# Optimization experiments

Measured on AMD Instinct MI355X. Metric: run time of the kernel, lower is better.

Reference implementation:

```python
import jax, jax.numpy as jnp
import numpy as np

B, S, D = 4, 2048, 1024
H = 16
HD = D // H
DFF = 4096
MAX_REL = 32
EPS = 1e-5


def _rms_norm(x, w):
    rms = jnp.sqrt(jnp.mean(x * x, axis=-1, keepdims=True) + EPS)
    return x / rms * w


def setup_inputs() -> dict:
    key = jax.random.key(0)
    ks = jax.random.split(key, 16)
    sc = 0.02
    d = {
        "x": jax.random.normal(ks[0], (B, S, D), dtype=jnp.float32),
        "g1": jnp.ones((D,), dtype=jnp.float32),
        "g2": jnp.ones((D,), dtype=jnp.float32),
        "wq": jax.random.normal(ks[1], (D, D), dtype=jnp.float32) * sc,
        "bq": jnp.zeros((D,), dtype=jnp.float32),
        "wk": jax.random.normal(ks[2], (D, D), dtype=jnp.float32) * sc,
        "bk": jnp.zeros((D,), dtype=jnp.float32),
        "wv": jax.random.normal(ks[3], (D, D), dtype=jnp.float32) * sc,
        "bv": jnp.zeros((D,), dtype=jnp.float32),
        "wo": jax.random.normal(ks[4], (D, D), dtype=jnp.float32) * sc,
        "bo": jnp.zeros((D,), dtype=jnp.float32),
        "rel_pos": jax.random.normal(ks[5], (H, 2 * MAX_REL + 1), dtype=jnp.float32),
        "w1": jax.random.normal(ks[6], (D, DFF), dtype=jnp.float32) * sc,
        "b1": jnp.zeros((DFF,), dtype=jnp.float32),
        "w2": jax.random.normal(ks[7], (DFF, D), dtype=jnp.float32) * sc,
        "b2": jnp.zeros((D,), dtype=jnp.float32),
    }
    return d


def reference(x, g1, g2, wq, bq, wk, bk, wv, bv, wo, bo, rel_pos, w1, b1, w2, b2):
    b, s, d = x.shape
    # --- multi-head attention with relative-position bias ---
    q = (x @ wq + bq).reshape(b, s, H, HD).transpose(0, 2, 1, 3)  # [B,H,S,HD]
    k = (x @ wk + bk).reshape(b, s, H, HD).transpose(0, 2, 1, 3)
    v = (x @ wv + bv).reshape(b, s, H, HD).transpose(0, 2, 1, 3)
    scores = jnp.einsum("bhqd,bhkd->bhqk", q, k) / jnp.sqrt(jnp.float32(HD))
    # relative position bias: gather from (H, 2*MAX_REL+1) table
    pos = jnp.arange(s)
    rel = pos[None, :] - pos[:, None]                # [S,S]
    idx = jnp.clip(rel, -MAX_REL, MAX_REL) + MAX_REL  # [S,S]
    bias = rel_pos[:, idx]                            # [H,S,S]
    scores = scores + bias[None]
    attn = jax.nn.softmax(scores, axis=-1)
    out = jnp.einsum("bhqk,bhkd->bhqd", attn, v)
    out = out.transpose(0, 2, 1, 3).reshape(b, s, d)
    attn_out = out @ wo + bo
    # residual + RMSNorm
    x = _rms_norm(attn_out + x, g1)
    # --- feed-forward (exact GELU) ---
    h = jax.nn.gelu(x @ w1 + b1, approximate=False)
    ff = h @ w2 + b2
    x = _rms_norm(ff + x, g2)
    return x
```

## Files before the change

### kernel.cpp

```cpp
#include <hip/hip_runtime.h>

#define B_ 4
#define S_ 2048
#define D_ 1024
#define H_ 16
#define HD_ 64
#define DFF_ 4096
#define MR_ 32
#define M_ (B_*S_)

typedef unsigned short u16;
typedef __attribute__((ext_vector_type(8))) short bf16x8;
typedef __attribute__((ext_vector_type(4))) float f32x4;

#define MFMA16 __builtin_amdgcn_mfma_f32_16x16x32_bf16
#define A_CONST 0.18033688011112f
#define LOG2E_ 1.44269504088896f

__device__ __forceinline__ u16 f2b(float f) {
  unsigned u = __builtin_bit_cast(unsigned, f);
  u = u + 0x7FFFu + ((u >> 16) & 1u);
  return (u16)(u >> 16);
}
__device__ __forceinline__ float b2f(u16 h) {
  unsigned u = ((unsigned)h) << 16;
  return __builtin_bit_cast(float, u);
}
__device__ __forceinline__ float exp2_fast(float x) {
  float r;
  asm("v_exp_f32 %0, %1" : "=v"(r) : "v"(x));
  return r;
}
__device__ __forceinline__ unsigned cvtpk(float lo, float hi) {
  unsigned r;
  asm("v_cvt_pk_bf16_f32 %0, %1, %2" : "=v"(r) : "v"(lo), "v"(hi));
  return r;
}
__device__ __forceinline__ float max3f(float a, float b, float c) {
  float r;
  asm("v_max3_f32 %0, %1, %2, %3" : "=v"(r) : "v"(a), "v"(b), "v"(c));
  return r;
}
__device__ __forceinline__ int med3i(int a, int b, int c) {
  int r;
  asm("v_med3_i32 %0, %1, %2, %3" : "=v"(r) : "v"(a), "v"(b), "v"(c));
  return r;
}
__device__ __forceinline__ void gl_lds16(const void* g, void* l) {
  __builtin_amdgcn_global_load_lds(
      (const __attribute__((address_space(1))) void*)g,
      (__attribute__((address_space(3))) void*)l, 16, 0, 0);
}

#define SWZ(r) ((((((r)>>3)&1)<<2) ^ ((r)&7)) << 4)
#define SWZ64(r) ((((r)>>1)&3) << 4)

__global__ __launch_bounds__(256) void cvt_kernel(const float* __restrict__ in,
                                                  u16* __restrict__ out, int n4) {
  int i = blockIdx.x * 256 + threadIdx.x;
  if (i < n4) {
    float4 v = ((const float4*)in)[i];
    ushort4 o;
    o.x = f2b(v.x); o.y = f2b(v.y); o.z = f2b(v.z); o.w = f2b(v.w);
    ((ushort4*)out)[i] = o;
  }
}

__global__ __launch_bounds__(256) void wtrans_kernel(const float* __restrict__ in,
                                                     u16* __restrict__ out, int R, int C) {
  __shared__ float t[32][33];
  int c0 = blockIdx.x * 32, r0 = blockIdx.y * 32;
  int x = threadIdx.x, y = threadIdx.y;
#pragma unroll
  for (int i = 0; i < 4; ++i)
    t[y + i*8][x] = in[(long)(r0 + y + i*8) * C + c0 + x];
  __syncthreads();
#pragma unroll
  for (int i = 0; i < 4; ++i)
    out[(long)(c0 + y + i*8) * R + r0 + x] = f2b(t[x][y + i*8]);
}

__global__ __launch_bounds__(256) void vtrans_kernel(const u16* __restrict__ v,
                                                     u16* __restrict__ vT) {
  __shared__ u16 t[32][33];
  int bh = blockIdx.y; int b = bh >> 4, h = bh & 15;
  int s0 = (blockIdx.x >> 1) * 32;
  int d0 = (blockIdx.x & 1) * 32;
  int x = threadIdx.x, y = threadIdx.y;
#pragma unroll
  for (int i = 0; i < 4; ++i)
    t[y + i*8][x] = v[((long)(b*S_ + s0 + y + i*8)) * D_ + h*64 + d0 + x];
  __syncthreads();
#pragma unroll
  for (int i = 0; i < 4; ++i)
    vT[((long)((b*H_ + h)*HD_ + d0 + y + i*8)) * S_ + s0 + x] = t[x][y + i*8];
}

template<int EPI, int WN>
__global__ __launch_bounds__(512, 2) void gemm9(
    const u16* __restrict__ A, const u16* __restrict__ BT,
    const float* __restrict__ bias0, const float* __restrict__ bias1,
    const float* __restrict__ bias2,
    u16* __restrict__ C0, u16* __restrict__ C1, u16* __restrict__ C2,
    int Ndim, int Kdim)
{
  constexpr int BN = WN * 64;
  constexpr int WM = 8 / WN;
  constexpr int MROWS = 256 / WM;
  constexpr int MF = MROWS / 16;
  __shared__ char lds[4][32768];
  const int tid = threadIdx.x;
  const int w = tid >> 6, lane = tid & 63;
  const int lr = lane & 15, lg = lane >> 4;
  const int wm = w / WN, wn = w % WN;

  const int nbx = Ndim / BN;
  const int cpx = gridDim.x >> 3;
  const int bid = blockIdx.x;
  const int swzb = (bid & 7) * cpx + (bid >> 3);
  const long blockM = (long)(swzb / nbx) * 256;
  const long blockN = (long)(swzb % nbx) * BN;

  const int srow = tid >> 2;
  const int scol = ((tid & 3) * 16) ^ SWZ64(srow);
  const u16* Ag  = A + (blockM + srow) * (long)Kdim + (scol >> 1);
  const u16* Ag2 = Ag + (long)128 * Kdim;
  const u16* Bg  = BT + (blockN + srow) * (long)Kdim + (scol >> 1);
  const u16* Bg2 = Bg + (long)128 * Kdim;
  char* const ldsAw = &lds[0][0] + w * 1024;
  char* const ldsBw = &lds[0][0] + 16384 + w * 1024;

#define STAGE_A(t) { char* d_=ldsAw+((t)&3)*32768; const long ko_=(long)(t)*32; \
    gl_lds16(Ag  + ko_, d_); gl_lds16(Ag2 + ko_, d_ + 8192); }
#define STAGE_B(t) { char* d_=ldsBw+((t)&3)*32768; const long ko_=(long)(t)*32; \
    gl_lds16(Bg  + ko_, d_); if constexpr (WN==4) gl_lds16(Bg2 + ko_, d_ + 8192); }

  const int rsw = (lg * 16) ^ SWZ64(lr);
  int offA[MF], offB[4];
#pragma unroll
  for (int mf = 0; mf < MF; ++mf) offA[mf] = (wm*MROWS + mf*16 + lr) * 64 + rsw;
#pragma unroll
  for (int nf = 0; nf < 4; ++nf)  offB[nf] = 16384 + (wn*64 + nf*16 + lr) * 64 + rsw;

  f32x4 acc[MF][4] = {};
  const int NS = Kdim >> 5;

  STAGE_A(0); STAGE_B(0); STAGE_A(1); STAGE_B(1);
  if (WN == 4) asm volatile("s_waitcnt vmcnt(4)" ::: "memory");
  else         asm volatile("s_waitcnt vmcnt(3)" ::: "memory");
  __builtin_amdgcn_s_barrier();

  for (int t = 0; t < NS; ++t) {
    const char* sl = &lds[t & 3][0];
    bf16x8 af[MF], bfr[4];
    if constexpr (WN == 4) {
#pragma unroll
      for (int mf = 0; mf < MF; ++mf) af[mf] = *(const bf16x8*)(sl + offA[mf]);
      bfr[0] = *(const bf16x8*)(sl + offB[0]);
      bfr[1] = *(const bf16x8*)(sl + offB[1]);
      if (t + 2 < NS) STAGE_A(t + 2);
      __builtin_amdgcn_s_barrier();
      __builtin_amdgcn_s_setprio(1);
#pragma unroll
      for (int mf = 0; mf < MF; ++mf) acc[mf][0] = MFMA16(bfr[0], af[mf], acc[mf][0], 0, 0, 0);
#pragma unroll
      for (int mf = 0; mf < MF; ++mf) acc[mf][1] = MFMA16(bfr[1], af[mf], acc[mf][1], 0, 0, 0);
      __builtin_amdgcn_s_setprio(0);
      __builtin_amdgcn_s_barrier();
      bfr[2] = *(const bf16x8*)(sl + offB[2]);
      bfr[3] = *(const bf16x8*)(sl + offB[3]);
      if (t + 2 < NS) {
        STAGE_B(t + 2);
        asm volatile("s_waitcnt vmcnt(4)" ::: "memory");
      } else if (t == NS - 2) {
        asm volatile("s_waitcnt vmcnt(0)" ::: "memory");
      }
      __builtin_amdgcn_s_barrier();
      __builtin_amdgcn_s_setprio(1);
#pragma unroll
      for (int mf = 0; mf < MF; ++mf) acc[mf][2] = MFMA16(bfr[2], af[mf], acc[mf][2], 0, 0, 0);
#pragma unroll
      for (int mf = 0; mf < MF; ++mf) acc[mf][3] = MFMA16(bfr[3], af[mf], acc[mf][3], 0, 0, 0);
      __builtin_amdgcn_s_setprio(0);
      __builtin_amdgcn_s_barrier();
    } else {
#pragma unroll
      for (int mf = 0; mf < MF; ++mf) af[mf] = *(const bf16x8*)(sl + offA[mf]);
#pragma unroll
      for (int nf = 0; nf < 4; ++nf)  bfr[nf] = *(const bf16x8*)(sl + offB[nf]);
      if (t + 2 < NS) {
        STAGE_A(t + 2); STAGE_B(t + 2);
        asm volatile("s_waitcnt vmcnt(3)" ::: "memory");
      } else if (t == NS - 2) {
        asm volatile("s_waitcnt vmcnt(0)" ::: "memory");
      }
      __builtin_amdgcn_s_barrier();
      __builtin_amdgcn_s_setprio(1);
#pragma unroll
      for (int mf = 0; mf < MF; ++mf)
#pragma unroll
        for (int nf = 0; nf < 4; ++nf)
          acc[mf][nf] = MFMA16(bfr[nf], af[mf], acc[mf][nf], 0, 0, 0);
      __builtin_amdgcn_s_setprio(0);
      __builtin_amdgcn_s_barrier();
    }
  }

  const float* bsel = bias0;
  u16* osel = C0;
  long nstride = Ndim;
  long ncol0 = blockN;
  if (EPI == 3) {
    int mat = (int)(blockN >> 10);
    bsel = mat == 0 ? bias0 : (mat == 1 ? bias1 : bias2);
    osel = mat == 0 ? C0 : (mat == 1 ? C1 : C2);
    nstride = 1024;
    ncol0 = blockN & 1023;
  }
  const long row0 = blockM + wm*MROWS;
#pragma unroll
  for (int mf = 0; mf < MF; ++mf) {
    long row = row0 + mf*16 + lr;
#pragma unroll
    for (int nf = 0; nf < 4; ++nf) {
      long col = ncol0 + wn*64 + nf*16 + lg*4;
      float4 bv = *(const float4*)&bsel[col];
      float v0 = acc[mf][nf][0] + bv.x;
      float v1 = acc[mf][nf][1] + bv.y;
      float v2 = acc[mf][nf][2] + bv.z;
      float v3 = acc[mf][nf][3] + bv.w;
      if (EPI == 2) {
        v0 = 0.5f*v0*(1.0f + erff(v0*0.70710678118654752f));
        v1 = 0.5f*v1*(1.0f + erff(v1*0.70710678118654752f));
        v2 = 0.5f*v2*(1.0f + erff(v2*0.70710678118654752f));
        v3 = 0.5f*v3*(1.0f + erff(v3*0.70710678118654752f));
      }
      ushort4 st;
      st.x = f2b(v0); st.y = f2b(v1); st.z = f2b(v2); st.w = f2b(v3);
      *(ushort4*)&osel[row * nstride + col] = st;
    }
  }
#undef STAGE_A
#undef STAGE_B
}

__device__ __forceinline__ float max16v(const f32x4* s) {
  float a = max3f(s[0][0], s[0][1], s[0][2]);
  float b = max3f(s[0][3], s[1][0], s[1][1]);
  float c = max3f(s[1][2], s[1][3], s[2][0]);
  float d = max3f(s[2][1], s[2][2], s[2][3]);
  float e = max3f(s[3][0], s[3][1], s[3][2]);
  float f = max3f(a, b, s[3][3]);
  float g = max3f(c, d, e);
  return fmaxf(f, g);
}
__device__ __forceinline__ float max16s(const float* v) {
  float a = max3f(v[0], v[1], v[2]);
  float b = max3f(v[3], v[4], v[5]);
  float c = max3f(v[6], v[7], v[8]);
  float d = max3f(v[9], v[10], v[11]);
  float e = max3f(v[12], v[13], v[14]);
  float f = max3f(a, b, v[15]);
  float g = max3f(c, d, e);
  return fmaxf(f, g);
}

__device__ __forceinline__ void sm_finish(float* p, float& l_r, bf16x8* pfo) {
  float ls = ((p[0]+p[1])+(p[2]+p[3])) + ((p[4]+p[5])+(p[6]+p[7]))
           + ((p[8]+p[9])+(p[10]+p[11])) + ((p[12]+p[13])+(p[14]+p[15]));
  ls += __shfl_xor(ls, 16);
  ls += __shfl_xor(ls, 32);
  l_r += ls;
#pragma unroll
  for (int ks = 0; ks < 2; ++ks) {
    uint4 uu;
    uu.x = cvtpk(p[ks*4+0], p[ks*4+1]);
    uu.y = cvtpk(p[ks*4+2], p[ks*4+3]);
    uu.z = cvtpk(p[(ks+2)*4+0], p[(ks+2)*4+1]);
    uu.w = cvtpk(p[(ks+2)*4+2], p[(ks+2)*4+3]);
    pfo[ks] = __builtin_bit_cast(bf16x8, uu);
  }
}

__device__ __forceinline__ void softmax_uni(const f32x4* s, float bu,
    float& m_r, float& l_r, f32x4* acc, bf16x8* pfo)
{
  float mx = fmaf(max16v(s), A_CONST, bu);
  mx = fmaxf(mx, __shfl_xor(mx, 16));
  mx = fmaxf(mx, __shfl_xor(mx, 32));
  if (!__all(mx <= m_r + 8.0f)) {
    float mn = fmaxf(m_r, mx);
    float sc = exp2_fast(m_r - mn);
    m_r = mn;
    l_r *= sc;
#pragma unroll
    for (int ni = 0; ni < 4; ++ni) acc[ni] *= sc;
  }
  float cc = bu - m_r;
  float p[16];
#pragma unroll
  for (int ni = 0; ni < 4; ++ni)
#pragma unroll
    for (int j = 0; j < 4; ++j)
      p[ni*4+j] = exp2_fast(fmaf(s[ni][j], A_CONST, cc));
  sm_finish(p, l_r, pfo);
}

__device__ __forceinline__ void softmax_slow(const f32x4* s, const float* relb,
    int rbase, float& m_r, float& l_r, f32x4* acc, bf16x8* pfo)
{
  float sv[16];
#pragma unroll
  for (int ni = 0; ni < 4; ++ni) {
    const int koff = (ni&1)*32 + (ni>>1)*4;
#pragma unroll
    for (int j = 0; j < 4; ++j) {
      int idx = med3i(rbase + koff + j + MR_, 0, 2*MR_);
      sv[ni*4+j] = fmaf(s[ni][j], A_CONST, relb[idx]);
    }
  }
  float mx = max16s(sv);
  mx = fmaxf(mx, __shfl_xor(mx, 16));
  mx = fmaxf(mx, __shfl_xor(mx, 32));
  if (!__all(mx <= m_r + 8.0f)) {
    float mn = fmaxf(m_r, mx);
    float sc = exp2_fast(m_r - mn);
    m_r = mn;
    l_r *= sc;
#pragma unroll
    for (int ni = 0; ni < 4; ++ni) acc[ni] *= sc;
  }
  float p[16];
#pragma unroll
  for (int i = 0; i < 16; ++i) p[i] = exp2_fast(sv[i] - m_r);
  sm_finish(p, l_r, pfo);
}

__global__ __launch_bounds__(256, 4) void attn3_kernel(
    const u16* __restrict__ q, const u16* __restrict__ k,
    const u16* __restrict__ vT, const float* __restrict__ rel_pos,
    u16* __restrict__ ao)
{
  __shared__ u16 KB[2][4096];
  __shared__ u16 VB[2][4096];
  __shared__ float relb[2*MR_ + 1];

  const int tid = threadIdx.x;
  const int w = tid >> 6, lane = tid & 63;
  const int lr = lane & 15, lg = lane >> 4;
  const int qt = blockIdx.x, bh = blockIdx.y;
  const int b = bh >> 4, h = bh & 15;
  const int q0 = qt * 128;
  const int qq = q0 + w*32;

  if (tid < 2*MR_ + 1) relb[tid] = rel_pos[h * (2*MR_ + 1) + tid] * LOG2E_;

  const int srow0 = w*8 + (lane >> 3);
  const int srow1 = 32 + srow0;
  const int scb   = (lane & 7) * 16;
  const int col0  = scb ^ SWZ(srow0);
  const int col1  = scb ^ SWZ(srow1);

  const long qkbase = ((long)(b*S_)) * D_ + h*64;
  const long vbase  = ((long)((b*H_ + h) * HD_)) * S_;

  {
    const u16* qg = q + qkbase + (long)q0 * D_;
#pragma unroll
    for (int c = 0; c < 4; ++c) {
      int row = c*32 + srow0;
      int colc = scb ^ SWZ(row);
      gl_lds16(qg + (long)row*D_ + (colc >> 1), &KB[0][0] + (c*32 + w*8)*64);
    }
  }
  __syncthreads();
  bf16x8 qf[4];
#pragma unroll
  for (int qi = 0; qi < 2; ++qi)
#pragma unroll
    for (int ks = 0; ks < 2; ++ks) {
      int row = w*32 + qi*16 + lr;
      qf[qi*2+ks] = *(const bf16x8*)((const char*)&KB[0][0] + row*128 + ((ks*64 + lg*16) ^ SWZ(row)));
    }
  const float bHI = relb[2*MR_];
  const float bLO = relb[0];
  __syncthreads();

  int offK0[4], offV0[4];
#pragma unroll
  for (int ni = 0; ni < 4; ++ni) {
    int kr = (ni&1)*32 + (lr>>2)*8 + (ni>>1)*4 + (lr&3);
    int vr = ni*16 + lr;
    offK0[ni] = kr*128 + ((lg*16) ^ SWZ(kr));
    offV0[ni] = vr*128 + ((lg*16) ^ SWZ(vr));
  }

  const u16* kp0 = k  + qkbase + (long)srow0*D_ + (col0 >> 1);
  const u16* kp1 = k  + qkbase + (long)srow1*D_ + (col1 >> 1);
  const u16* vp0 = vT + vbase  + (long)srow0*S_ + (col0 >> 1);
  const u16* vp1 = vT + vbase  + (long)srow1*S_ + (col1 >> 1);
  u16* kb_w0 = &KB[0][(w*8)*64];
  u16* kb_w1 = &KB[0][(32 + w*8)*64];
  u16* vb_w0 = &VB[0][(w*8)*64];
  u16* vb_w1 = &VB[0][(32 + w*8)*64];

  float m_r[2] = {-1e30f, -1e30f};
  float l_r[2] = {0.f, 0.f};
  f32x4 acco[2][4] = {};

  gl_lds16(kp0, kb_w0);
  gl_lds16(kp1, kb_w1);
  gl_lds16(vp0, vb_w0);
  gl_lds16(vp1, vb_w1);

  const long kstep = (long)64 * D_;
  const int NT = S_ / 64;
  for (int t = 0; t < NT; ++t) {
    const int cur = t & 1;
    __syncthreads();
    if (t + 1 < NT) {
      int bufo = (cur ^ 1) * 4096;
      gl_lds16(kp0 + (long)(t+1)*kstep, kb_w0 + bufo);
      gl_lds16(kp1 + (long)(t+1)*kstep, kb_w1 + bufo);
      gl_lds16(vp0 + (t+1)*64, vb_w0 + bufo);
      gl_lds16(vp1 + (t+1)*64, vb_w1 + bufo);
    }
    const char* Kb = (const char*)&KB[cur][0];
    const char* Vb = (const char*)&VB[cur][0];
    const int k0 = t * 64;

    f32x4 s0[4] = {}, s1[4] = {};
#pragma unroll
    for (int ks = 0; ks < 2; ++ks)
#pragma unroll
      for (int ni = 0; ni < 4; ++ni) {
        bf16x8 kf = *(const bf16x8*)(Kb + (offK0[ni] ^ (ks*64)));
        s0[ni] = MFMA16(kf, qf[ks],   s0[ni], 0, 0, 0);
        s1[ni] = MFMA16(kf, qf[2+ks], s1[ni], 0, 0, 0);
      }

    bf16x8 pf0[2], pf1[2];
    bool hi_u = (k0 - (qq + 31)) >= MR_;
    bool lo_u = (qq - (k0 + 63)) >= MR_;
    if (hi_u || lo_u) {
      float bu = hi_u ? bHI : bLO;
      softmax_uni(s0, bu, m_r[0], l_r[0], acco[0], pf0);
      softmax_uni(s1, bu, m_r[1], l_r[1], acco[1], pf1);
    } else {
      int rb0 = k0 + lg*8 - (qq + lr);
      softmax_slow(s0, relb, rb0,      m_r[0], l_r[0], acco[0], pf0);
      softmax_slow(s1, relb, rb0 - 16, m_r[1], l_r[1], acco[1], pf1);
    }

#pragma unroll
    for (int ks = 0; ks < 2; ++ks)
#pragma unroll
      for (int ni = 0; ni < 4; ++ni) {
        bf16x8 vf = *(const bf16x8*)(Vb + (offV0[ni] ^ (ks*64)));
        acco[0][ni] = MFMA16(vf, pf0[ks], acco[0][ni], 0, 0, 0);
        acco[1][ni] = MFMA16(vf, pf1[ks], acco[1][ni], 0, 0, 0);
      }
  }

#pragma unroll
  for (int qi = 0; qi < 2; ++qi) {
    float inv = 1.0f / l_r[qi];
    long orow = ((long)(b*S_ + qq + qi*16 + lr)) * D_ + h*64;
#pragma unroll
    for (int ni = 0; ni < 4; ++ni) {
      ushort4 ov;
      ov.x = f2b(acco[qi][ni][0] * inv);
      ov.y = f2b(acco[qi][ni][1] * inv);
      ov.z = f2b(acco[qi][ni][2] * inv);
      ov.w = f2b(acco[qi][ni][3] * inv);
      *(ushort4*)(ao + orow + ni*16 + lg*4) = ov;
    }
  }
}

template<int ABF, int BBF>
__global__ __launch_bounds__(256) void rmsnorm_kernel(
    const void* __restrict__ a, const void* __restrict__ b,
    const float* __restrict__ g, float* __restrict__ outf,
    u16* __restrict__ outb)
{
  long row = blockIdx.x;
  int tid = threadIdx.x;
  float ya[4], yb[4], y[4];
  if (ABF) {
    ushort4 av = ((const ushort4*)a)[row*256 + tid];
    ya[0] = b2f(av.x); ya[1] = b2f(av.y); ya[2] = b2f(av.z); ya[3] = b2f(av.w);
  } else {
    float4 av = ((const float4*)a)[row*256 + tid];
    ya[0] = av.x; ya[1] = av.y; ya[2] = av.z; ya[3] = av.w;
  }
  if (BBF) {
    ushort4 bv = ((const ushort4*)b)[row*256 + tid];
    yb[0] = b2f(bv.x); yb[1] = b2f(bv.y); yb[2] = b2f(bv.z); yb[3] = b2f(bv.w);
  } else {
    float4 bv = ((const float4*)b)[row*256 + tid];
    yb[0] = bv.x; yb[1] = bv.y; yb[2] = bv.z; yb[3] = bv.w;
  }
  float ss = 0.f;
#pragma unroll
  for (int i = 0; i < 4; ++i) { y[i] = ya[i] + yb[i]; ss += y[i]*y[i]; }
#pragma unroll
  for (int m = 1; m < 64; m <<= 1) ss += __shfl_xor(ss, m);
  __shared__ float red[4];
  int w = tid >> 6, lane = tid & 63;
  if (lane == 0) red[w] = ss;
  __syncthreads();
  ss = red[0] + red[1] + red[2] + red[3];
  float rinv = rsqrtf(ss * (1.0f / D_) + 1e-5f);
  float4 gv = ((const float4*)g)[tid];
  float o[4] = { y[0]*rinv*gv.x, y[1]*rinv*gv.y, y[2]*rinv*gv.z, y[3]*rinv*gv.w };
  if (outf) {
    float4 of = { o[0], o[1], o[2], o[3] };
    ((float4*)outf)[row*256 + tid] = of;
  }
  if (outb) {
    ushort4 ob;
    ob.x = f2b(o[0]); ob.y = f2b(o[1]); ob.z = f2b(o[2]); ob.w = f2b(o[3]);
    ((ushort4*)outb)[row*256 + tid] = ob;
  }
}

extern "C" void kernel_launch(void* const* d_in, const int* in_sizes, int n_in,
                              void* d_out, int out_size, void* d_ws, size_t ws_size,
                              hipStream_t stream) {
  const float* x   = (const float*)d_in[0];
  const float* g1  = (const float*)d_in[1];
  const float* g2  = (const float*)d_in[2];
  const float* wq  = (const float*)d_in[3];
  const float* bq  = (const float*)d_in[4];
  const float* wk  = (const float*)d_in[5];
  const float* bk  = (const float*)d_in[6];
  const float* wv  = (const float*)d_in[7];
  const float* bv  = (const float*)d_in[8];
  const float* wo  = (const float*)d_in[9];
  const float* bo  = (const float*)d_in[10];
  const float* rel = (const float*)d_in[11];
  const float* w1  = (const float*)d_in[12];
  const float* b1  = (const float*)d_in[13];
  const float* w2  = (const float*)d_in[14];
  const float* b2  = (const float*)d_in[15];
  float* out = (float*)d_out;

  char* ws = (char*)d_ws;
  const size_t MB = 1024ull * 1024ull;
  u16* xb   = (u16*)(ws + 0);
  u16* wqT  = (u16*)(ws + 16*MB);
  u16* wkT  = (u16*)(ws + 18*MB);
  u16* wvT  = (u16*)(ws + 20*MB);
  u16* woT  = (u16*)(ws + 22*MB);
  u16* w1T  = (u16*)(ws + 24*MB);
  u16* w2T  = (u16*)(ws + 32*MB);
  u16* qb   = (u16*)(ws + 40*MB);
  u16* kb   = (u16*)(ws + 56*MB);
  u16* vb   = (u16*)(ws + 72*MB);
  u16* vTb  = (u16*)(ws + 88*MB);
  u16* aob  = (u16*)(ws + 104*MB);
  u16* prjb = (u16*)(ws + 120*MB);
  u16* x1b  = (u16*)(ws + 136*MB);
  u16* hb   = (u16*)(ws + 40*MB);
  u16* ffb  = (u16*)(ws + 120*MB);
  (void)ws_size; (void)in_sizes; (void)n_in; (void)out_size;

  dim3 tb(32, 8);

  cvt_kernel<<<M_*D_/4/256, 256, 0, stream>>>(x, xb, M_*D_/4);
  wtrans_kernel<<<dim3(D_/32,   D_/32),   tb, 0, stream>>>(wq, wqT, D_,   D_);
  wtrans_kernel<<<dim3(D_/32,   D_/32),   tb, 0, stream>>>(wk, wkT, D_,   D_);
  wtrans_kernel<<<dim3(D_/32,   D_/32),   tb, 0, stream>>>(wv, wvT, D_,   D_);
  wtrans_kernel<<<dim3(D_/32,   D_/32),   tb, 0, stream>>>(wo, woT, D_,   D_);
  wtrans_kernel<<<dim3(DFF_/32, D_/32),   tb, 0, stream>>>(w1, w1T, D_,   DFF_);
  wtrans_kernel<<<dim3(D_/32,   DFF_/32), tb, 0, stream>>>(w2, w2T, DFF_, D_);

  gemm9<3,4><<<(3072/256)*(M_/256), 512, 0, stream>>>(
      xb, wqT, bq, bk, bv, qb, kb, vb, 3072, D_);

  vtrans_kernel<<<dim3((S_/32)*(HD_/32), B_*H_), tb, 0, stream>>>(vb, vTb);

  attn3_kernel<<<dim3(S_/128, B_*H_), 256, 0, stream>>>(qb, kb, vTb, rel, aob);

  gemm9<0,2><<<(D_/128)*(M_/256), 512, 0, stream>>>(
      aob, woT, bo, nullptr, nullptr, prjb, nullptr, nullptr, D_, D_);

  rmsnorm_kernel<1,0><<<M_, 256, 0, stream>>>(prjb, x, g1, nullptr, x1b);

  gemm9<2,4><<<(DFF_/256)*(M_/256), 512, 0, stream>>>(
      x1b, w1T, b1, nullptr, nullptr, hb, nullptr, nullptr, DFF_, D_);

  gemm9<0,2><<<(D_/128)*(M_/256), 512, 0, stream>>>(
      hb, w2T, b2, nullptr, nullptr, ffb, nullptr, nullptr, D_, DFF_);

  rmsnorm_kernel<1,1><<<M_, 256, 0, stream>>>(ffb, x1b, g2, out, nullptr);
}
```

Before: 450.5 us.

## Shrink WN=4 GEMM tile to 128 rows, triple-buffer LDS, stage epilogue through LDS

The GEMM is reworked. The WN=4 variants (QKV and FFN1) now use a 128x256 tile instead of 256x256, so the grid doubles. The LDS ring drops from four fixed 32KB slots to three slots sized to the tile, and the split-phase WN=4 loop is unified into a single loop with one stage per iteration. The epilogue now writes bf16 results into swizzled LDS and then emits coalesced 16-byte row stores to global memory, replacing scattered 8-byte stores. The aims are better occupancy, wave balance and store coalescing. In exchange each A element is loaded more often (less reuse per tile) and there is an extra barrier plus an LDS round-trip.

```diff
diff --git a/kernel.cpp b/kernel.cpp
--- a/kernel.cpp
+++ b/kernel.cpp
@@ -97,18 +97,17 @@
 }
 
 template<int EPI, int WN>
-__global__ __launch_bounds__(512, 2) void gemm9(
+__global__ __launch_bounds__(512, 2) void gemm10(
     const u16* __restrict__ A, const u16* __restrict__ BT,
     const float* __restrict__ bias0, const float* __restrict__ bias1,
     const float* __restrict__ bias2,
     u16* __restrict__ C0, u16* __restrict__ C1, u16* __restrict__ C2,
     int Ndim, int Kdim)
 {
+  constexpr int BM = (WN == 4) ? 128 : 256;
   constexpr int BN = WN * 64;
-  constexpr int WM = 8 / WN;
-  constexpr int MROWS = 256 / WM;
-  constexpr int MF = MROWS / 16;
-  __shared__ char lds[4][32768];
+  constexpr int SLOT = (BM + BN) * 64;
+  __shared__ char lds[3 * SLOT];
   const int tid = threadIdx.x;
   const int w = tid >> 6, lane = tid & 63;
   const int lr = lane & 15, lg = lane >> 4;
@@ -118,92 +117,64 @@
   const int cpx = gridDim.x >> 3;
   const int bid = blockIdx.x;
   const int swzb = (bid & 7) * cpx + (bid >> 3);
-  const long blockM = (long)(swzb / nbx) * 256;
+  const long blockM = (long)(swzb / nbx) * BM;
   const long blockN = (long)(swzb % nbx) * BN;
 
   const int srow = tid >> 2;
   const int scol = ((tid & 3) * 16) ^ SWZ64(srow);
-  const u16* Ag  = A + (blockM + srow) * (long)Kdim + (scol >> 1);
+  const u16* Ag  = A  + (blockM + srow) * (long)Kdim + (scol >> 1);
   const u16* Ag2 = Ag + (long)128 * Kdim;
   const u16* Bg  = BT + (blockN + srow) * (long)Kdim + (scol >> 1);
   const u16* Bg2 = Bg + (long)128 * Kdim;
-  char* const ldsAw = &lds[0][0] + w * 1024;
-  char* const ldsBw = &lds[0][0] + 16384 + w * 1024;
-
-#define STAGE_A(t) { char* d_=ldsAw+((t)&3)*32768; const long ko_=(long)(t)*32; \
-    gl_lds16(Ag  + ko_, d_); gl_lds16(Ag2 + ko_, d_ + 8192); }
-#define STAGE_B(t) { char* d_=ldsBw+((t)&3)*32768; const long ko_=(long)(t)*32; \
-    gl_lds16(Bg  + ko_, d_); if constexpr (WN==4) gl_lds16(Bg2 + ko_, d_ + 8192); }
+
+  auto STAGE = [&](int slot, long ko) {
+    char* base = &lds[slot * SLOT];
+    gl_lds16(Ag + ko, base + w * 1024);
+    if constexpr (WN == 2) gl_lds16(Ag2 + ko, base + 8192 + w * 1024);
+    gl_lds16(Bg + ko, base + BM * 64 + w * 1024);
+    if constexpr (WN == 4) gl_lds16(Bg2 + ko, base + BM * 64 + 8192 + w * 1024);
+  };
 
   const int rsw = (lg * 16) ^ SWZ64(lr);
-  int offA[MF], offB[4];
-#pragma unroll
-  for (int mf = 0; mf < MF; ++mf) offA[mf] = (wm*MROWS + mf*16 + lr) * 64 + rsw;
-#pragma unroll
-  for (int nf = 0; nf < 4; ++nf)  offB[nf] = 16384 + (wn*64 + nf*16 + lr) * 64 + rsw;
-
-  f32x4 acc[MF][4] = {};
+  int offA[4], offB[4];
+#pragma unroll
+  for (int mf = 0; mf < 4; ++mf) offA[mf] = (wm*64 + mf*16 + lr) * 64 + rsw;
+#pragma unroll
+  for (int nf = 0; nf < 4; ++nf) offB[nf] = BM*64 + (wn*64 + nf*16 + lr) * 64 + rsw;
+
+  f32x4 acc[4][4] = {};
   const int NS = Kdim >> 5;
 
-  STAGE_A(0); STAGE_B(0); STAGE_A(1); STAGE_B(1);
-  if (WN == 4) asm volatile("s_waitcnt vmcnt(4)" ::: "memory");
-  else         asm volatile("s_waitcnt vmcnt(3)" ::: "memory");
+  STAGE(0, 0);
+  STAGE(1, 32);
+  asm volatile("s_waitcnt vmcnt(3)" ::: "memory");
   __builtin_amdgcn_s_barrier();
 
+  int sl = 0, sl2 = 2;
   for (int t = 0; t < NS; ++t) {
-    const char* sl = &lds[t & 3][0];
-    bf16x8 af[MF], bfr[4];
-    if constexpr (WN == 4) {
-#pragma unroll
-      for (int mf = 0; mf < MF; ++mf) af[mf] = *(const bf16x8*)(sl + offA[mf]);
-      bfr[0] = *(const bf16x8*)(sl + offB[0]);
-      bfr[1] = *(const bf16x8*)(sl + offB[1]);
-      if (t + 2 < NS) STAGE_A(t + 2);
-      __builtin_amdgcn_s_barrier();
-      __builtin_amdgcn_s_setprio(1);
-#pragma unroll
-      for (int mf = 0; mf < MF; ++mf) acc[mf][0] = MFMA16(bfr[0], af[mf], acc[mf][0], 0, 0, 0);
-#pragma unroll
-      for (int mf = 0; mf < MF; ++mf) acc[mf][1] = MFMA16(bfr[1], af[mf], acc[mf][1], 0, 0, 0);
-      __builtin_amdgcn_s_setprio(0);
-      __builtin_amdgcn_s_barrier();
-      bfr[2] = *(const bf16x8*)(sl + offB[2]);
-      bfr[3] = *(const bf16x8*)(sl + offB[3]);
-      if (t + 2 < NS) {
-        STAGE_B(t + 2);
-        asm volatile("s_waitcnt vmcnt(4)" ::: "memory");
-      } else if (t == NS - 2) {
-        asm volatile("s_waitcnt vmcnt(0)" ::: "memory");
-      }
-      __builtin_amdgcn_s_barrier();
-      __builtin_amdgcn_s_setprio(1);
-#pragma unroll
-      for (int mf = 0; mf < MF; ++mf) acc[mf][2] = MFMA16(bfr[2], af[mf], acc[mf][2], 0, 0, 0);
-#pragma unroll
-      for (int mf = 0; mf < MF; ++mf) acc[mf][3] = MFMA16(bfr[3], af[mf], acc[mf][3], 0, 0, 0);
-      __builtin_amdgcn_s_setprio(0);
-      __builtin_amdgcn_s_barrier();
-    } else {
-#pragma unroll
-      for (int mf = 0; mf < MF; ++mf) af[mf] = *(const bf16x8*)(sl + offA[mf]);
-#pragma unroll
-      for (int nf = 0; nf < 4; ++nf)  bfr[nf] = *(const bf16x8*)(sl + offB[nf]);
-      if (t + 2 < NS) {
-        STAGE_A(t + 2); STAGE_B(t + 2);
-        asm volatile("s_waitcnt vmcnt(3)" ::: "memory");
-      } else if (t == NS - 2) {
-        asm volatile("s_waitcnt vmcnt(0)" ::: "memory");
-      }
-      __builtin_amdgcn_s_barrier();
-      __builtin_amdgcn_s_setprio(1);
-#pragma unroll
-      for (int mf = 0; mf < MF; ++mf)
-#pragma unroll
-        for (int nf = 0; nf < 4; ++nf)
-          acc[mf][nf] = MFMA16(bfr[nf], af[mf], acc[mf][nf], 0, 0, 0);
-      __builtin_amdgcn_s_setprio(0);
-      __builtin_amdgcn_s_barrier();
-    }
+    const char* s = &lds[sl * SLOT];
+    bf16x8 af[4], bfr[4];
+#pragma unroll
+    for (int mf = 0; mf < 4; ++mf) af[mf] = *(const bf16x8*)(s + offA[mf]);
+#pragma unroll
+    for (int nf = 0; nf < 4; ++nf) bfr[nf] = *(const bf16x8*)(s + offB[nf]);
+    if (t + 2 < NS) {
+      STAGE(sl2, (long)(t + 2) * 32);
+      asm volatile("s_waitcnt vmcnt(3)" ::: "memory");
+    } else if (t == NS - 2) {
+      asm volatile("s_waitcnt vmcnt(0)" ::: "memory");
+    }
+    __builtin_amdgcn_s_barrier();
+    __builtin_amdgcn_s_setprio(1);
+#pragma unroll
+    for (int mf = 0; mf < 4; ++mf)
+#pragma unroll
+      for (int nf = 0; nf < 4; ++nf)
+        acc[mf][nf] = MFMA16(bfr[nf], af[mf], acc[mf][nf], 0, 0, 0);
+    __builtin_amdgcn_s_setprio(0);
+    __builtin_amdgcn_s_barrier();
+    sl  = (sl  == 2) ? 0 : sl  + 1;
+    sl2 = (sl2 == 2) ? 0 : sl2 + 1;
   }
 
   const float* bsel = bias0;
@@ -217,14 +188,15 @@
     nstride = 1024;
     ncol0 = blockN & 1023;
   }
-  const long row0 = blockM + wm*MROWS;
-#pragma unroll
-  for (int mf = 0; mf < MF; ++mf) {
-    long row = row0 + mf*16 + lr;
+  constexpr int RB = BN * 2;
+  char* const et = &lds[0];
+#pragma unroll
+  for (int mf = 0; mf < 4; ++mf) {
+    const int row = wm*64 + mf*16 + lr;
 #pragma unroll
     for (int nf = 0; nf < 4; ++nf) {
-      long col = ncol0 + wn*64 + nf*16 + lg*4;
-      float4 bv = *(const float4*)&bsel[col];
+      const int colu = wn*64 + nf*16 + lg*4;
+      float4 bv = *(const float4*)&bsel[ncol0 + colu];
       float v0 = acc[mf][nf][0] + bv.x;
       float v1 = acc[mf][nf][1] + bv.y;
       float v2 = acc[mf][nf][2] + bv.z;
@@ -237,11 +209,20 @@
       }
       ushort4 st;
       st.x = f2b(v0); st.y = f2b(v1); st.z = f2b(v2); st.w = f2b(v3);
-      *(ushort4*)&osel[row * nstride + col] = st;
-    }
-  }
-#undef STAGE_A
-#undef STAGE_B
+      *(ushort4*)(et + row*RB + ((colu*2) ^ ((row & 7) << 4))) = st;
+    }
+  }
+  __syncthreads();
+  constexpr int CHR  = RB / 16;
+  constexpr int ITER = BM * CHR / 512;
+#pragma unroll
+  for (int i = 0; i < ITER; ++i) {
+    const int idx = i*512 + tid;
+    const int row = idx / CHR;
+    const int cb  = (idx % CHR) * 16;
+    uint4 val = *(const uint4*)(et + row*RB + (cb ^ ((row & 7) << 4)));
+    *(uint4*)&osel[(blockM + row) * nstride + ncol0 + (cb >> 1)] = val;
+  }
 }
 
 __device__ __forceinline__ float max16v(const f32x4* s) {
@@ -576,22 +557,22 @@
   wtrans_kernel<<<dim3(DFF_/32, D_/32),   tb, 0, stream>>>(w1, w1T, D_,   DFF_);
   wtrans_kernel<<<dim3(D_/32,   DFF_/32), tb, 0, stream>>>(w2, w2T, DFF_, D_);
 
-  gemm9<3,4><<<(3072/256)*(M_/256), 512, 0, stream>>>(
+  gemm10<3,4><<<(3072/256)*(M_/128), 512, 0, stream>>>(
       xb, wqT, bq, bk, bv, qb, kb, vb, 3072, D_);
 
   vtrans_kernel<<<dim3((S_/32)*(HD_/32), B_*H_), tb, 0, stream>>>(vb, vTb);
 
   attn3_kernel<<<dim3(S_/128, B_*H_), 256, 0, stream>>>(qb, kb, vTb, rel, aob);
 
-  gemm9<0,2><<<(D_/128)*(M_/256), 512, 0, stream>>>(
+  gemm10<0,2><<<(D_/128)*(M_/256), 512, 0, stream>>>(
       aob, woT, bo, nullptr, nullptr, prjb, nullptr, nullptr, D_, D_);
 
   rmsnorm_kernel<1,0><<<M_, 256, 0, stream>>>(prjb, x, g1, nullptr, x1b);
 
-  gemm9<2,4><<<(DFF_/256)*(M_/256), 512, 0, stream>>>(
+  gemm10<2,4><<<(DFF_/256)*(M_/128), 512, 0, stream>>>(
       x1b, w1T, b1, nullptr, nullptr, hb, nullptr, nullptr, DFF_, D_);
 
-  gemm9<0,2><<<(D_/128)*(M_/256), 512, 0, stream>>>(
+  gemm10<0,2><<<(D_/128)*(M_/256), 512, 0, stream>>>(
       hb, w2T, b2, nullptr, nullptr, ffb, nullptr, nullptr, D_, DFF_);
 
   rmsnorm_kernel<1,1><<<M_, 256, 0, stream>>>(ffb, x1b, g2, out, nullptr);
```

Result: faster. 433.9 us (-3.7%).
